# Kernel tuning notes

Measured on AMD Instinct MI355X. Metric: run time of the kernel, lower is better.

Reference implementation:

```python
import jax, jax.numpy as jnp
import numpy as np


def setup_inputs() -> dict:
    key = jax.random.key(0)
    k0, k1, k2, k3 = jax.random.split(key, 4)
    B, T, C = 4, 2048, 1024
    x = jax.random.normal(k0, (B, T, C), dtype=jnp.float32)
    s = C ** -0.5  # init-scale for weights so activations stay O(1)
    Wq = jax.random.normal(k1, (C, C), dtype=jnp.float32) * s
    Wk = jax.random.normal(k2, (C, C), dtype=jnp.float32) * s
    Wv = jax.random.normal(k3, (C, C), dtype=jnp.float32) * s
    return {"x": x, "Wq": Wq, "Wk": Wk, "Wv": Wv}


def reference(x, Wq, Wk, Wv):
    B, T, C = x.shape
    # torch nn.Linear: y = x @ W.T
    q = jnp.einsum('btc,dc->btd', x, Wq)
    k = jnp.einsum('btc,dc->btd', x, Wk)
    v = jnp.einsum('btc,dc->btd', x, Wv)
    scale = C ** -0.5
    wei = jnp.einsum('btd,bsd->bts', q, k) * scale  # [B, T, T]
    causal = jnp.tril(jnp.ones((T, T), dtype=bool))
    wei = jnp.where(causal, wei, -jnp.inf)
    wei = jax.nn.softmax(wei, axis=-1)
    out = jnp.einsum('bts,bsd->btd', wei, v)
    return out
```

## Files before the change

### kernel.cpp

```cpp
#include <hip/hip_runtime.h>
#include <hip/hip_bf16.h>
#include <math.h>

#define B_ 4
#define T_ 2048
#define C_ 1024
#define M_ (B_*T_)

typedef __attribute__((ext_vector_type(8))) __bf16 bf16x8;
typedef __attribute__((ext_vector_type(4))) float floatx4;

__device__ inline float bf2f(unsigned short u){
    return __uint_as_float(((unsigned)u) << 16);
}
__device__ inline unsigned short f2bf(float f){
    unsigned u = __float_as_uint(f);
    unsigned r = (u + 0x7fffu + ((u >> 16) & 1u)) >> 16;
    return (unsigned short)r;
}

__device__ inline void llds16(const unsigned short* g, unsigned short* lds){
    __builtin_amdgcn_global_load_lds(
        (const __attribute__((address_space(1))) unsigned int*)g,
        (__attribute__((address_space(3))) unsigned int*)(unsigned int)(uintptr_t)lds,
        16, 0, 0);
}

#define NX_ (M_*C_/4)
#define NW_ (C_*C_/4)
#define NL4_ (M_/4)
__global__ __launch_bounds__(256) void cast_all(
    const float* __restrict__ x, const float* __restrict__ wq,
    const float* __restrict__ wk, const float* __restrict__ wv,
    unsigned short* __restrict__ xb, unsigned short* __restrict__ wb,
    float* __restrict__ l)
{
    int i = blockIdx.x * 256 + threadIdx.x;
    const float* src; unsigned short* dst; int idx;
    if (i < NX_){ src = x; dst = xb; idx = i; }
    else if (i < NX_ + 3 * NW_){
        i -= NX_;
        int w = i / NW_; idx = i - w * NW_;
        src = (w == 0) ? wq : ((w == 1) ? wk : wv);
        dst = wb + (size_t)w * C_ * C_;
    } else {
        ((float4*)l)[i - NX_ - 3 * NW_] = make_float4(0.f, 0.f, 0.f, 0.f);
        return;
    }
    float4 v = ((const float4*)src)[idx];
    ((ushort4*)dst)[idx] = make_ushort4(f2bf(v.x), f2bf(v.y), f2bf(v.z), f2bf(v.w));
}

template<int WM, int WN>
__device__ inline void gemm_core(const unsigned short* __restrict__ A,
                                 const unsigned short* __restrict__ Bm,
                                 int lda, int ldb, int m0, int n0, int kTiles,
                                 unsigned short* As, unsigned short* Bs,
                                 floatx4 (*acc)[WN/16])
{
    const int tid  = threadIdx.x;
    const int lane = tid & 63;
    const int wave = tid >> 6;
    const int wm = (wave >> 1) * WM;
    const int wn = (wave & 1) * WN;
    const int fr = lane & 15;
    const int fq = lane >> 4;
    const int cxor = fr & 7;
    const int sr = lane >> 3;
    const int sc = ((lane & 7) ^ ((lane >> 3) & 7)) * 8;

    const unsigned short* gA = A  + (size_t)(m0 + wave * (WM/2) + sr) * lda + sc;
    const unsigned short* gB = Bm + (size_t)(n0 + wave * (WN/2) + sr) * ldb + sc;
    unsigned short* ldsA = As + wave * (WM/2) * 64;
    unsigned short* ldsB = Bs + wave * (WN/2) * 64;

    for (int kt = 0; kt < kTiles; kt++){
        const int k0 = kt * 64;
        __syncthreads();
        #pragma unroll
        for (int i = 0; i < WM/16; i++)
            llds16(gA + (size_t)(i * 8) * lda + k0, ldsA + i * 8 * 64);
        #pragma unroll
        for (int i = 0; i < WN/16; i++)
            llds16(gB + (size_t)(i * 8) * ldb + k0, ldsB + i * 8 * 64);
        __syncthreads();
        #pragma unroll
        for (int ks = 0; ks < 64; ks += 32){
            const int cpos = (((ks >> 3) + fq) ^ cxor) * 8;
            bf16x8 af[WM/16], bv[WN/16];
            #pragma unroll
            for (int i = 0; i < WM/16; i++)
                af[i] = *(const bf16x8*)(As + (wm + i*16 + fr) * 64 + cpos);
            #pragma unroll
            for (int j = 0; j < WN/16; j++)
                bv[j] = *(const bf16x8*)(Bs + (wn + j*16 + fr) * 64 + cpos);
            #pragma unroll
            for (int i = 0; i < WM/16; i++)
                #pragma unroll
                for (int j = 0; j < WN/16; j++)
                    acc[i][j] = __builtin_amdgcn_mfma_f32_16x16x32_bf16(af[i], bv[j], acc[i][j], 0, 0, 0);
        }
    }
}

__global__ __launch_bounds__(256, 4) void proj_gemm(
    const unsigned short* __restrict__ xb,
    const unsigned short* __restrict__ Wb,
    unsigned short* __restrict__ Qb, unsigned short* __restrict__ Kb,
    unsigned short* __restrict__ Vt, int h)
{
    __shared__ unsigned short As[128 * 64];
    __shared__ unsigned short Bs[128 * 64];
    const int L = blockIdx.x;
    const int k = L & 7, j = L >> 3;
    const int m0 = (k * 8 + (j & 7)) * 128;
    const int n0 = (((j >> 3) & 3) + h * 4) * 128;
    const int z  = j >> 5;
    const unsigned short* W = Wb + (size_t)z * C_ * C_;

    floatx4 acc[4][4];
    #pragma unroll
    for (int i = 0; i < 4; i++)
        #pragma unroll
        for (int jj = 0; jj < 4; jj++) acc[i][jj] = (floatx4){0.f,0.f,0.f,0.f};
    gemm_core<64, 64>(xb, W, C_, C_, m0, n0, C_ / 64, As, Bs, acc);

    const int lane = threadIdx.x & 63, wave = threadIdx.x >> 6;
    const int wm = (wave >> 1) * 64, wn = (wave & 1) * 64;
    const int fr = lane & 15, fq = lane >> 4;

    if (z < 2){
        unsigned short* Y = z ? Kb : Qb;
        #pragma unroll
        for (int i = 0; i < 4; i++)
            #pragma unroll
            for (int jj = 0; jj < 4; jj++)
                #pragma unroll
                for (int r = 0; r < 4; r++){
                    int row = m0 + wm + i*16 + fq*4 + r;
                    int col = n0 + wn + jj*16 + fr;
                    Y[(size_t)row * C_ + col] = f2bf(acc[i][jj][r]);
                }
    } else {
        #pragma unroll
        for (int i = 0; i < 4; i++)
            #pragma unroll
            for (int jj = 0; jj < 4; jj++){
                int row = m0 + wm + i*16 + fq*4;
                int col = n0 + wn + jj*16 + fr;
                int b = row / T_, t = row % T_;
                ushort4 o = make_ushort4(f2bf(acc[i][jj][0]), f2bf(acc[i][jj][1]),
                                         f2bf(acc[i][jj][2]), f2bf(acc[i][jj][3]));
                *(ushort4*)&Vt[(size_t)b * C_ * T_ + (size_t)col * T_ + t] = o;
            }
    }
}

__global__ __launch_bounds__(256, 4) void score_gemm(
    const unsigned short* __restrict__ Qb, const unsigned short* __restrict__ Kb,
    unsigned short* __restrict__ P, float* __restrict__ l)
{
    const int L = blockIdx.x;
    const int k = L & 7, j = L >> 3;
    const int b = j / 34, rem = j % 34;
    const int th = rem & 1, rr = rem >> 1;
    int ti, si;
    if (rr <= 15 - k){ ti = 15 - k; si = rr; }
    else             { ti = k;      si = rr - (16 - k); }
    const int t0 = ti * 128 + th * 64, s0 = si * 128;

    __shared__ unsigned short As[64 * 64];
    __shared__ unsigned short Bs[128 * 64];
    floatx4 acc[2][4];
    #pragma unroll
    for (int i = 0; i < 2; i++)
        #pragma unroll
        for (int jj = 0; jj < 4; jj++) acc[i][jj] = (floatx4){0.f,0.f,0.f,0.f};
    gemm_core<32, 64>(Qb + (size_t)b * T_ * C_, Kb + (size_t)b * T_ * C_,
                      C_, C_, t0, s0, C_ / 64, As, Bs, acc);

    const int lane = threadIdx.x & 63, wave = threadIdx.x >> 6;
    const int wm = (wave >> 1) * 32, wn = (wave & 1) * 64;
    const int fr = lane & 15, fq = lane >> 4;
    unsigned short* Pb = P + (size_t)b * T_ * T_;
    const float scale = 0.03125f;
    float rsl[2][4];
    #pragma unroll
    for (int i = 0; i < 2; i++)
        #pragma unroll
        for (int r2 = 0; r2 < 4; r2++) rsl[i][r2] = 0.f;

    #pragma unroll
    for (int i = 0; i < 2; i++)
        #pragma unroll
        for (int jj = 0; jj < 4; jj++)
            #pragma unroll
            for (int r2 = 0; r2 < 4; r2++){
                int t = t0 + wm + i*16 + fq*4 + r2;
                int s = s0 + wn + jj*16 + fr;
                float v = (s <= t) ? __expf(acc[i][jj][r2] * scale) : 0.f;
                rsl[i][r2] += v;
                Pb[(size_t)t * T_ + s] = f2bf(v);
            }
    #pragma unroll
    for (int i = 0; i < 2; i++)
        #pragma unroll
        for (int r2 = 0; r2 < 4; r2++){
            float v = rsl[i][r2];
            v += __shfl_xor(v, 1, 64);
            v += __shfl_xor(v, 2, 64);
            v += __shfl_xor(v, 4, 64);
            v += __shfl_xor(v, 8, 64);
            if (fr == 0){
                int t = t0 + wm + i*16 + fq*4 + r2;
                atomicAdd(&l[(size_t)b * T_ + t], v);
            }
        }
}

__global__ __launch_bounds__(256, 4) void pv_gemm(
    const unsigned short* __restrict__ P, const unsigned short* __restrict__ Vt,
    const float* __restrict__ l, float* __restrict__ out)
{
    const int L = blockIdx.x;
    const int k = L & 7, j = L >> 3;
    const int b = j >> 4;
    const int n0 = (j & 15) * 64;

    __shared__ unsigned short As[128 * 64];
    __shared__ unsigned short Bs[64 * 64];

    const int lane = threadIdx.x & 63, wave = threadIdx.x >> 6;
    const int wm = (wave >> 1) * 64, wn = (wave & 1) * 32;
    const int fr = lane & 15, fq = lane >> 4;
    float* ob = out + (size_t)b * T_ * C_;
    const float* lb = l + (size_t)b * T_;

    #pragma unroll
    for (int phase = 0; phase < 2; phase++){
        const int ti = phase ? k : (15 - k);
        const int t0 = ti * 128;
        const int kTiles = 2 * (ti + 1);

        floatx4 acc[4][2];
        #pragma unroll
        for (int i = 0; i < 4; i++)
            #pragma unroll
            for (int jj = 0; jj < 2; jj++) acc[i][jj] = (floatx4){0.f,0.f,0.f,0.f};
        gemm_core<64, 32>(P + (size_t)b * T_ * T_, Vt + (size_t)b * C_ * T_,
                          T_, T_, t0, n0, kTiles, As, Bs, acc);

        #pragma unroll
        for (int i = 0; i < 4; i++){
            float inv[4];
            #pragma unroll
            for (int r2 = 0; r2 < 4; r2++)
                inv[r2] = 1.f / lb[t0 + wm + i*16 + fq*4 + r2];
            #pragma unroll
            for (int jj = 0; jj < 2; jj++)
                #pragma unroll
                for (int r2 = 0; r2 < 4; r2++){
                    int t = t0 + wm + i*16 + fq*4 + r2;
                    int d = n0 + wn + jj*16 + fr;
                    ob[(size_t)t * C_ + d] = acc[i][jj][r2] * inv[r2];
                }
        }
    }
}

extern "C" void kernel_launch(void* const* d_in, const int* in_sizes, int n_in,
                              void* d_out, int out_size, void* d_ws, size_t ws_size,
                              hipStream_t stream)
{
    const float* x  = (const float*)d_in[0];
    const float* Wq = (const float*)d_in[1];
    const float* Wk = (const float*)d_in[2];
    const float* Wv = (const float*)d_in[3];
    float* out = (float*)d_out;

    unsigned short* Qb = (unsigned short*)d_ws;
    unsigned short* Kb = Qb + (size_t)M_ * C_;
    unsigned short* Vt = Kb + (size_t)M_ * C_;
    unsigned short* P  = Vt + (size_t)M_ * C_;
    float* l = (float*)(P + (size_t)M_ * T_);
    unsigned short* xb = P;
    unsigned short* Wb = P + (size_t)M_ * C_;

    cast_all<<<(NX_ + 3 * NW_ + NL4_ + 255) / 256, 256, 0, stream>>>(
        x, Wq, Wk, Wv, xb, Wb, l);
    proj_gemm <<<768, 256, 0, stream>>>(xb, Wb, Qb, Kb, Vt, 0);
    proj_gemm <<<768, 256, 0, stream>>>(xb, Wb, Qb, Kb, Vt, 1);
    score_gemm<<<1088, 256, 0, stream>>>(Qb, Kb, P, l);
    pv_gemm   <<<512,  256, 0, stream>>>(P, Vt, l, out);
}
```

Baseline: 210.8 us.

## Retile score and PV GEMMs to 64x64 blocks and merge projection launches

The two projection launches become one 1536-block launch covering all eight N tiles. The score and PV kernels move from hand-balanced 1D grids with 128-row tiles to plain 3D grids of 64x64 tiles. Score blocks above the diagonal return early, and each PV block handles a single row tile with a causal K range, at higher occupancy bounds. This aims for more parallelism and fewer launches, but it cuts operand reuse per block and drops the previous causal load balancing.

```diff
diff --git a/kernel.cpp b/kernel.cpp
--- a/kernel.cpp
+++ b/kernel.cpp
@@ -107,15 +107,15 @@
     const unsigned short* __restrict__ xb,
     const unsigned short* __restrict__ Wb,
     unsigned short* __restrict__ Qb, unsigned short* __restrict__ Kb,
-    unsigned short* __restrict__ Vt, int h)
+    unsigned short* __restrict__ Vt)
 {
     __shared__ unsigned short As[128 * 64];
     __shared__ unsigned short Bs[128 * 64];
     const int L = blockIdx.x;
     const int k = L & 7, j = L >> 3;
     const int m0 = (k * 8 + (j & 7)) * 128;
-    const int n0 = (((j >> 3) & 3) + h * 4) * 128;
-    const int z  = j >> 5;
+    const int n0 = ((j >> 3) & 7) * 128;
+    const int z  = j >> 6;
     const unsigned short* W = Wb + (size_t)z * C_ * C_;
 
     floatx4 acc[4][4];
@@ -156,31 +156,26 @@
     }
 }
 
-__global__ __launch_bounds__(256, 4) void score_gemm(
+__global__ __launch_bounds__(256, 8) void score_gemm(
     const unsigned short* __restrict__ Qb, const unsigned short* __restrict__ Kb,
     unsigned short* __restrict__ P, float* __restrict__ l)
 {
-    const int L = blockIdx.x;
-    const int k = L & 7, j = L >> 3;
-    const int b = j / 34, rem = j % 34;
-    const int th = rem & 1, rr = rem >> 1;
-    int ti, si;
-    if (rr <= 15 - k){ ti = 15 - k; si = rr; }
-    else             { ti = k;      si = rr - (16 - k); }
-    const int t0 = ti * 128 + th * 64, s0 = si * 128;
+    const int si = blockIdx.x, ti = blockIdx.y, b = blockIdx.z;
+    if (si > ti) return;
+    const int t0 = ti * 64, s0 = si * 64;
 
     __shared__ unsigned short As[64 * 64];
-    __shared__ unsigned short Bs[128 * 64];
-    floatx4 acc[2][4];
-    #pragma unroll
-    for (int i = 0; i < 2; i++)
-        #pragma unroll
-        for (int jj = 0; jj < 4; jj++) acc[i][jj] = (floatx4){0.f,0.f,0.f,0.f};
-    gemm_core<32, 64>(Qb + (size_t)b * T_ * C_, Kb + (size_t)b * T_ * C_,
+    __shared__ unsigned short Bs[64 * 64];
+    floatx4 acc[2][2];
+    #pragma unroll
+    for (int i = 0; i < 2; i++)
+        #pragma unroll
+        for (int jj = 0; jj < 2; jj++) acc[i][jj] = (floatx4){0.f,0.f,0.f,0.f};
+    gemm_core<32, 32>(Qb + (size_t)b * T_ * C_, Kb + (size_t)b * T_ * C_,
                       C_, C_, t0, s0, C_ / 64, As, Bs, acc);
 
     const int lane = threadIdx.x & 63, wave = threadIdx.x >> 6;
-    const int wm = (wave >> 1) * 32, wn = (wave & 1) * 64;
+    const int wm = (wave >> 1) * 32, wn = (wave & 1) * 32;
     const int fr = lane & 15, fq = lane >> 4;
     unsigned short* Pb = P + (size_t)b * T_ * T_;
     const float scale = 0.03125f;
@@ -193,7 +188,7 @@
     #pragma unroll
     for (int i = 0; i < 2; i++)
         #pragma unroll
-        for (int jj = 0; jj < 4; jj++)
+        for (int jj = 0; jj < 2; jj++)
             #pragma unroll
             for (int r2 = 0; r2 < 4; r2++){
                 int t = t0 + wm + i*16 + fq*4 + r2;
@@ -218,53 +213,45 @@
         }
 }
 
-__global__ __launch_bounds__(256, 4) void pv_gemm(
+__global__ __launch_bounds__(256, 8) void pv_gemm(
     const unsigned short* __restrict__ P, const unsigned short* __restrict__ Vt,
     const float* __restrict__ l, float* __restrict__ out)
 {
-    const int L = blockIdx.x;
-    const int k = L & 7, j = L >> 3;
-    const int b = j >> 4;
-    const int n0 = (j & 15) * 64;
-
-    __shared__ unsigned short As[128 * 64];
+    const int d = blockIdx.x, ti = blockIdx.y, b = blockIdx.z;
+    const int t0 = ti * 64;
+    const int n0 = d * 64;
+
+    __shared__ unsigned short As[64 * 64];
     __shared__ unsigned short Bs[64 * 64];
 
+    floatx4 acc[2][2];
+    #pragma unroll
+    for (int i = 0; i < 2; i++)
+        #pragma unroll
+        for (int jj = 0; jj < 2; jj++) acc[i][jj] = (floatx4){0.f,0.f,0.f,0.f};
+    gemm_core<32, 32>(P + (size_t)b * T_ * T_, Vt + (size_t)b * C_ * T_,
+                      T_, T_, t0, n0, ti + 1, As, Bs, acc);
+
     const int lane = threadIdx.x & 63, wave = threadIdx.x >> 6;
-    const int wm = (wave >> 1) * 64, wn = (wave & 1) * 32;
+    const int wm = (wave >> 1) * 32, wn = (wave & 1) * 32;
     const int fr = lane & 15, fq = lane >> 4;
     float* ob = out + (size_t)b * T_ * C_;
     const float* lb = l + (size_t)b * T_;
 
     #pragma unroll
-    for (int phase = 0; phase < 2; phase++){
-        const int ti = phase ? k : (15 - k);
-        const int t0 = ti * 128;
-        const int kTiles = 2 * (ti + 1);
-
-        floatx4 acc[4][2];
-        #pragma unroll
-        for (int i = 0; i < 4; i++)
-            #pragma unroll
-            for (int jj = 0; jj < 2; jj++) acc[i][jj] = (floatx4){0.f,0.f,0.f,0.f};
-        gemm_core<64, 32>(P + (size_t)b * T_ * T_, Vt + (size_t)b * C_ * T_,
-                          T_, T_, t0, n0, kTiles, As, Bs, acc);
-
-        #pragma unroll
-        for (int i = 0; i < 4; i++){
-            float inv[4];
-            #pragma unroll
-            for (int r2 = 0; r2 < 4; r2++)
-                inv[r2] = 1.f / lb[t0 + wm + i*16 + fq*4 + r2];
-            #pragma unroll
-            for (int jj = 0; jj < 2; jj++)
-                #pragma unroll
-                for (int r2 = 0; r2 < 4; r2++){
-                    int t = t0 + wm + i*16 + fq*4 + r2;
-                    int d = n0 + wn + jj*16 + fr;
-                    ob[(size_t)t * C_ + d] = acc[i][jj][r2] * inv[r2];
-                }
-        }
+    for (int i = 0; i < 2; i++){
+        float inv[4];
+        #pragma unroll
+        for (int r2 = 0; r2 < 4; r2++)
+            inv[r2] = 1.f / lb[t0 + wm + i*16 + fq*4 + r2];
+        #pragma unroll
+        for (int jj = 0; jj < 2; jj++)
+            #pragma unroll
+            for (int r2 = 0; r2 < 4; r2++){
+                int t = t0 + wm + i*16 + fq*4 + r2;
+                int dd = n0 + wn + jj*16 + fr;
+                ob[(size_t)t * C_ + dd] = acc[i][jj][r2] * inv[r2];
+            }
     }
 }
 
@@ -288,8 +275,7 @@
 
     cast_all<<<(NX_ + 3 * NW_ + NL4_ + 255) / 256, 256, 0, stream>>>(
         x, Wq, Wk, Wv, xb, Wb, l);
-    proj_gemm <<<768, 256, 0, stream>>>(xb, Wb, Qb, Kb, Vt, 0);
-    proj_gemm <<<768, 256, 0, stream>>>(xb, Wb, Qb, Kb, Vt, 1);
-    score_gemm<<<1088, 256, 0, stream>>>(Qb, Kb, P, l);
-    pv_gemm   <<<512,  256, 0, stream>>>(P, Vt, l, out);
-}
+    proj_gemm <<<1536, 256, 0, stream>>>(xb, Wb, Qb, Kb, Vt);
+    score_gemm<<<dim3(32, 32, 4), 256, 0, stream>>>(Qb, Kb, P, l);
+    pv_gemm   <<<dim3(16, 32, 4), 256, 0, stream>>>(P, Vt, l, out);
+}
```

Measured after the change: 242.5 us. 15.0% more time.
